# Optimization experiments

Measured on AMD Instinct MI355X. Metric: run time of the kernel, lower is better.

Reference implementation:

```python
import jax, jax.numpy as jnp
import numpy as np

B = 32          # batch_size
S = 64          # num_subgraph
D = 8           # dim_multi_hot (module-level global in source repo)
NE = S * D      # num_edges = 512
NNODES = 1024
E = 150000      # incidence rows
IN_UNITS = [16, 32, 32]
OUT_UNITS = [32, 32, 16]


def _glorot(key, shape):
    # glorot_normal over last two dims (out, in)
    fan_out, fan_in = shape[-2], shape[-1]
    std = (2.0 / (fan_in + fan_out)) ** 0.5
    return std * jax.random.normal(key, shape, dtype=jnp.float32)


def setup_inputs() -> dict:
    key = jax.random.key(0)
    ks = jax.random.split(key, 10)
    nodes_features = jax.random.normal(ks[0], (NNODES * S, IN_UNITS[0]), dtype=jnp.float32)
    c0 = jax.random.randint(ks[1], (E,), 0, B, dtype=jnp.int32)
    c1 = jax.random.randint(ks[2], (E,), 0, NNODES, dtype=jnp.int32)
    c2 = jax.random.randint(ks[3], (E,), 0, S, dtype=jnp.int32)
    c3 = jax.random.randint(ks[4], (E,), 0, D, dtype=jnp.int32)
    incidence_matrix = jnp.stack([c0, c1, c2, c3], axis=1)
    return {
        'nodes_features': nodes_features,
        'in_core0': _glorot(ks[5], (NE, IN_UNITS[1], IN_UNITS[0])),
        'in_bias0': jnp.zeros((NE, IN_UNITS[1], 1), jnp.float32),
        'in_core1': _glorot(ks[6], (NE, IN_UNITS[2], IN_UNITS[1])),
        'in_bias1': jnp.zeros((NE, IN_UNITS[2], 1), jnp.float32),
        'out_core0': _glorot(ks[7], (NE, OUT_UNITS[1], OUT_UNITS[0])),
        'out_bias0': jnp.zeros((NE, OUT_UNITS[1], 1), jnp.float32),
        'out_core1': _glorot(ks[8], (NE, OUT_UNITS[2], OUT_UNITS[1])),
        'out_bias1': jnp.zeros((NE, OUT_UNITS[2], 1), jnp.float32),
        'incidence_matrix': incidence_matrix,
    }


def reference(nodes_features, in_core0, in_bias0, in_core1, in_bias1,
              out_core0, out_bias0, out_core1, out_bias1, incidence_matrix):
    c0 = incidence_matrix[:, 0]
    c1 = incidence_matrix[:, 1]
    c2 = incidence_matrix[:, 2]
    c3 = incidence_matrix[:, 3]

    # gather node features per incidence row: [E, in0]
    x = nodes_features[c1 * S + c2]
    eidx = c2 * D + c3  # per-edge weight index, < NE

    # per-edge MLP (gathered batched matmul + bias + relu)
    for W, b in ((in_core0, in_bias0), (in_core1, in_bias1)):
        x = jax.nn.relu(jnp.einsum('eoi,ei->eo', W[eidx], x) + b[eidx, :, 0])

    # unsorted segment mean over irregular edge groups
    seg = c0 * (D * S) + c2 * D + c3
    nseg = B * S * D
    sums = jax.ops.segment_sum(x, seg, num_segments=nseg)           # [B*NE, 32]
    cnt = jax.ops.segment_sum(jnp.ones((x.shape[0], 1), x.dtype), seg, num_segments=nseg)
    ef = jnp.where(cnt > 0, sums / jnp.maximum(cnt, 1.0), 0.0)       # [B*NE, 32]

    # output MLP: weights tiled over batch (einsum avoids explicit repeat)
    ef = ef.reshape(B, NE, -1)
    for W, b in ((out_core0, out_bias0), (out_core1, out_bias1)):
        ef = jax.nn.relu(jnp.einsum('eoi,bei->beo', W, ef) + b[None, :, :, 0])

    return ef.reshape(B * NE, OUT_UNITS[-1], 1)
```

## Files before the change

kernel.cpp:

```cpp
#include <hip/hip_runtime.h>

#define B_    32
#define S_    64
#define D_    8
#define NE_   512
#define E_    150000
#define CAP   448
#define CSTRIDE 16

#define BMETA_BYTE_OFF   (NE_ * CSTRIDE * 4)
#define XSTAGE_BYTE_OFF  (BMETA_BYTE_OFF + NE_ * CAP * 4)

typedef __attribute__((ext_vector_type(8)))  short  short8;
typedef __attribute__((ext_vector_type(16))) float  float16;

__device__ __forceinline__ unsigned short f2bf(float f) {
    union { float f; unsigned int u; } cv; cv.f = f;
    unsigned int u = cv.u;
    return (unsigned short)((u + 0x7fffu + ((u >> 16) & 1u)) >> 16);
}
__device__ __forceinline__ unsigned int pack2bf(float a, float b) {
    return (unsigned int)f2bf(a) | ((unsigned int)f2bf(b) << 16);
}

__global__ __launch_bounds__(1024)
void scatter_stage_kernel(const int* __restrict__ inc,
                          const float* __restrict__ nf,
                          int* __restrict__ cursor,
                          int* __restrict__ bmeta,
                          uint4* __restrict__ xstage) {
    __shared__ int lcount[NE_];
    __shared__ int lbase[NE_];
    const int tid = threadIdx.x;

    for (int i = tid; i < NE_; i += 1024) lcount[i] = 0;
    __syncthreads();

    const int e = blockIdx.x * 1024 + tid;
    int ei = -1, lp = 0, b = 0, row = 0;
    if (e < E_) {
        const int4 c = ((const int4*)inc)[e];
        ei  = c.z * D_ + c.w;
        b   = c.x;
        row = c.y * S_ + c.z;
        lp  = atomicAdd(&lcount[ei], 1);
    }
    __syncthreads();
    for (int i = tid; i < NE_; i += 1024) {
        const int c = lcount[i];
        lbase[i] = (c > 0) ? atomicAdd(&cursor[i * CSTRIDE], c) : 0;
    }
    __syncthreads();
    if (ei >= 0) {
        const int idx = lbase[ei] + lp;
        if (idx < CAP) {
            const int slot = ei * CAP + idx;
            bmeta[slot] = b;
            const float4* xp = (const float4*)(nf + (size_t)row * 16);
            float4 v0 = xp[0], v1 = xp[1], v2 = xp[2], v3 = xp[3];
            uint4 pa, pb;
            pa.x = pack2bf(v0.x, v0.y); pa.y = pack2bf(v0.z, v0.w);
            pa.z = pack2bf(v1.x, v1.y); pa.w = pack2bf(v1.z, v1.w);
            pb.x = pack2bf(v2.x, v2.y); pb.y = pack2bf(v2.z, v2.w);
            pb.z = pack2bf(v3.x, v3.y); pb.w = pack2bf(v3.z, v3.w);
            xstage[slot * 2]     = pa;
            xstage[slot * 2 + 1] = pb;
        }
    }
}

#define HLP 40

__global__ __launch_bounds__(512, 4)
void main_mfma(const float* __restrict__ iw0, const float* __restrict__ ib0,
               const float* __restrict__ iw1, const float* __restrict__ ib1,
               const float* __restrict__ ow0, const float* __restrict__ ob0,
               const float* __restrict__ ow1, const float* __restrict__ ob1,
               const int* __restrict__ cursor, const int* __restrict__ bmeta,
               const uint4* __restrict__ xstage,
               float* __restrict__ out) {
    const int bid  = blockIdx.x;
    const int tid  = threadIdx.x;
    const int lane = tid & 63;
    const int wav  = tid >> 6;
    const int e32  = lane & 31;
    const int q    = lane >> 5;

    __shared__ float acc[32][33];
    __shared__ float hb[32][33];
    __shared__ float cnts[32];
    __shared__ float q0t[32 * 33];
    __shared__ float q1t[32 * 17];
    __shared__ float qb0s[32], qb1s[16];
    __shared__ unsigned short Hl[8][32 * HLP];

    short8 aWa, aWb0, aWb1;
    {
        const float* wa = iw0 + (size_t)bid * 512 + e32 * 16 + q * 8;
        float4 u0 = ((const float4*)wa)[0], u1 = ((const float4*)wa)[1];
        unsigned int p[4] = { pack2bf(u0.x,u0.y), pack2bf(u0.z,u0.w),
                              pack2bf(u1.x,u1.y), pack2bf(u1.z,u1.w) };
        aWa = *(short8*)p;
    }
    {
        const float* wb = iw1 + (size_t)bid * 1024 + e32 * 32 + q * 8;
        float4 u0 = ((const float4*)wb)[0], u1 = ((const float4*)wb)[1];
        unsigned int p[4] = { pack2bf(u0.x,u0.y), pack2bf(u0.z,u0.w),
                              pack2bf(u1.x,u1.y), pack2bf(u1.z,u1.w) };
        aWb0 = *(short8*)p;
        const float* wb2 = wb + 16;
        float4 u2 = ((const float4*)wb2)[0], u3 = ((const float4*)wb2)[1];
        unsigned int p2[4] = { pack2bf(u2.x,u2.y), pack2bf(u2.z,u2.w),
                               pack2bf(u3.x,u3.y), pack2bf(u3.z,u3.w) };
        aWb1 = *(short8*)p2;
    }
    float ba_r[16], bb_r[16];
    #pragma unroll
    for (int r = 0; r < 16; ++r) {
        const int o_r = (r & 3) + 8 * (r >> 2) + 4 * q;
        ba_r[r] = ib0[bid * 32 + o_r];
        bb_r[r] = ib1[bid * 32 + o_r];
    }

    for (int i = tid; i < 1024; i += 512) {
        const int o = i >> 5, k = i & 31;
        q0t[k * 33 + o] = ow0[(size_t)bid * 1024 + i];
    }
    { const int o = tid >> 5, k = tid & 31;
      q1t[k * 17 + o] = ow1[(size_t)bid * 512 + tid]; }
    if (tid < 32) { qb0s[tid] = ob0[bid * 32 + tid]; cnts[tid] = 0.f; }
    else if (tid < 48) qb1s[tid - 32] = ob1[bid * 16 + (tid - 32)];
    for (int i = tid; i < 32 * 33; i += 512) ((float*)acc)[i] = 0.f;
    __syncthreads();

    const int n = min(cursor[bid * CSTRIDE], CAP);
    const int ntiles = (n + 31) >> 5;
    const uint4* Xs = xstage + (size_t)bid * CAP * 2;
    const int*   Bm = bmeta + bid * CAP;
    unsigned short* hl = Hl[wav];

    for (int t = wav; t < ntiles; t += 8) {
        const int slot  = t * 32 + e32;
        const bool valid = slot < n;
        const int cs    = valid ? slot : (n - 1);

        short8 bX = *(const short8*)&Xs[cs * 2 + q];
        const int b_e = Bm[cs];

        float16 c0;
        #pragma unroll
        for (int r = 0; r < 16; ++r) c0[r] = ba_r[r];
        c0 = __builtin_amdgcn_mfma_f32_32x32x16_bf16(aWa, bX, c0, 0, 0, 0);

        #pragma unroll
        for (int r = 0; r < 16; r += 2) {
            const int o_r = (r & 3) + 8 * (r >> 2) + 4 * q;
            const unsigned int pk = pack2bf(fmaxf(c0[r], 0.f), fmaxf(c0[r + 1], 0.f));
            *(unsigned int*)(hl + e32 * HLP + o_r) = pk;
        }

        short8 bH0 = *(const short8*)(hl + e32 * HLP + q * 8);
        short8 bH1 = *(const short8*)(hl + e32 * HLP + 16 + q * 8);
        float16 c1;
        #pragma unroll
        for (int r = 0; r < 16; ++r) c1[r] = bb_r[r];
        c1 = __builtin_amdgcn_mfma_f32_32x32x16_bf16(aWb0, bH0, c1, 0, 0, 0);
        c1 = __builtin_amdgcn_mfma_f32_32x32x16_bf16(aWb1, bH1, c1, 0, 0, 0);

        if (valid) {
            #pragma unroll
            for (int r = 0; r < 16; ++r) {
                const int o_r = (r & 3) + 8 * (r >> 2) + 4 * q;
                atomicAdd(&acc[b_e][o_r], fmaxf(c1[r], 0.f));
            }
            if (q == 0) atomicAdd(&cnts[b_e], 1.f);
        }
    }
    __syncthreads();

    {
        const int b  = tid >> 4;
        const int j  = tid & 15;
        const float cv  = cnts[b];
        const float inv = cv > 0.f ? 1.0f / cv : 0.0f;
        #pragma unroll
        for (int s = 0; s < 2; ++s) {
            const int oo = j * 2 + s;
            float d = 0.f;
            #pragma unroll
            for (int k = 0; k < 32; ++k) d = fmaf(q0t[k * 33 + oo], acc[b][k], d);
            hb[b][oo] = fmaxf(fmaf(d, inv, qb0s[oo]), 0.f);
        }
    }
    __syncthreads();

    {
        const int b = tid >> 4;
        const int o = tid & 15;
        float d = qb1s[o];
        #pragma unroll
        for (int k = 0; k < 32; ++k) d = fmaf(q1t[k * 17 + o], hb[b][k], d);
        out[((size_t)b * NE_ + bid) * 16 + o] = fmaxf(d, 0.f);
    }
}

extern "C" void kernel_launch(void* const* d_in, const int* in_sizes, int n_in,
                              void* d_out, int out_size, void* d_ws, size_t ws_size,
                              hipStream_t stream) {
    const float* nf  = (const float*)d_in[0];
    const float* iw0 = (const float*)d_in[1];
    const float* ib0 = (const float*)d_in[2];
    const float* iw1 = (const float*)d_in[3];
    const float* ib1 = (const float*)d_in[4];
    const float* ow0 = (const float*)d_in[5];
    const float* ob0 = (const float*)d_in[6];
    const float* ow1 = (const float*)d_in[7];
    const float* ob1 = (const float*)d_in[8];
    const int*   inc = (const int*)d_in[9];

    int*   cursor = (int*)d_ws;
    int*   bmeta  = (int*)((char*)d_ws + BMETA_BYTE_OFF);
    uint4* xstage = (uint4*)((char*)d_ws + XSTAGE_BYTE_OFF);

    hipMemsetAsync(cursor, 0, NE_ * CSTRIDE * 4, stream);
    scatter_stage_kernel<<<(E_ + 1023) / 1024, 1024, 0, stream>>>(
        inc, nf, cursor, bmeta, xstage);
    main_mfma<<<NE_, 512, 0, stream>>>(iw0, ib0, iw1, ib1, ow0, ob0, ow1, ob1,
                                       cursor, bmeta, xstage, (float*)d_out);
}
```

Measured before the change: 123.9 us.

## Defer node feature gather to main kernel, scatter only packed index payload

```diff
diff --git a/kernel.cpp b/kernel.cpp
--- a/kernel.cpp
+++ b/kernel.cpp
@@ -8,8 +8,7 @@
 #define CAP   448
 #define CSTRIDE 16
 
-#define BMETA_BYTE_OFF   (NE_ * CSTRIDE * 4)
-#define XSTAGE_BYTE_OFF  (BMETA_BYTE_OFF + NE_ * CAP * 4)
+#define PAYLOAD_BYTE_OFF (NE_ * CSTRIDE * 4)
 
 typedef __attribute__((ext_vector_type(8)))  short  short8;
 typedef __attribute__((ext_vector_type(16))) float  float16;
@@ -24,11 +23,9 @@
 }
 
 __global__ __launch_bounds__(1024)
-void scatter_stage_kernel(const int* __restrict__ inc,
-                          const float* __restrict__ nf,
-                          int* __restrict__ cursor,
-                          int* __restrict__ bmeta,
-                          uint4* __restrict__ xstage) {
+void scatter_light(const int* __restrict__ inc,
+                   int* __restrict__ cursor,
+                   int* __restrict__ payload) {
     __shared__ int lcount[NE_];
     __shared__ int lbase[NE_];
     const int tid = threadIdx.x;
@@ -37,13 +34,12 @@
     __syncthreads();
 
     const int e = blockIdx.x * 1024 + tid;
-    int ei = -1, lp = 0, b = 0, row = 0;
+    int ei = -1, lp = 0, pl = 0;
     if (e < E_) {
         const int4 c = ((const int4*)inc)[e];
-        ei  = c.z * D_ + c.w;
-        b   = c.x;
-        row = c.y * S_ + c.z;
-        lp  = atomicAdd(&lcount[ei], 1);
+        ei = c.z * D_ + c.w;
+        pl = (c.x << 16) | (c.y * S_ + c.z);
+        lp = atomicAdd(&lcount[ei], 1);
     }
     __syncthreads();
     for (int i = tid; i < NE_; i += 1024) {
@@ -53,31 +49,19 @@
     __syncthreads();
     if (ei >= 0) {
         const int idx = lbase[ei] + lp;
-        if (idx < CAP) {
-            const int slot = ei * CAP + idx;
-            bmeta[slot] = b;
-            const float4* xp = (const float4*)(nf + (size_t)row * 16);
-            float4 v0 = xp[0], v1 = xp[1], v2 = xp[2], v3 = xp[3];
-            uint4 pa, pb;
-            pa.x = pack2bf(v0.x, v0.y); pa.y = pack2bf(v0.z, v0.w);
-            pa.z = pack2bf(v1.x, v1.y); pa.w = pack2bf(v1.z, v1.w);
-            pb.x = pack2bf(v2.x, v2.y); pb.y = pack2bf(v2.z, v2.w);
-            pb.z = pack2bf(v3.x, v3.y); pb.w = pack2bf(v3.z, v3.w);
-            xstage[slot * 2]     = pa;
-            xstage[slot * 2 + 1] = pb;
-        }
+        if (idx < CAP) payload[ei * CAP + idx] = pl;
     }
 }
 
 #define HLP 40
 
 __global__ __launch_bounds__(512, 4)
-void main_mfma(const float* __restrict__ iw0, const float* __restrict__ ib0,
+void main_mfma(const float* __restrict__ nf,
+               const float* __restrict__ iw0, const float* __restrict__ ib0,
                const float* __restrict__ iw1, const float* __restrict__ ib1,
                const float* __restrict__ ow0, const float* __restrict__ ob0,
                const float* __restrict__ ow1, const float* __restrict__ ob1,
-               const int* __restrict__ cursor, const int* __restrict__ bmeta,
-               const uint4* __restrict__ xstage,
+               const int* __restrict__ cursor, const int* __restrict__ payload,
                float* __restrict__ out) {
     const int bid  = blockIdx.x;
     const int tid  = threadIdx.x;
@@ -92,6 +76,7 @@
     __shared__ float q0t[32 * 33];
     __shared__ float q1t[32 * 17];
     __shared__ float qb0s[32], qb1s[16];
+    __shared__ float bias0s[32], bias1s[32];
     __shared__ unsigned short Hl[8][32 * HLP];
 
     short8 aWa, aWb0, aWb1;
@@ -114,13 +99,6 @@
                                pack2bf(u3.x,u3.y), pack2bf(u3.z,u3.w) };
         aWb1 = *(short8*)p2;
     }
-    float ba_r[16], bb_r[16];
-    #pragma unroll
-    for (int r = 0; r < 16; ++r) {
-        const int o_r = (r & 3) + 8 * (r >> 2) + 4 * q;
-        ba_r[r] = ib0[bid * 32 + o_r];
-        bb_r[r] = ib1[bid * 32 + o_r];
-    }
 
     for (int i = tid; i < 1024; i += 512) {
         const int o = i >> 5, k = i & 31;
@@ -128,15 +106,16 @@
     }
     { const int o = tid >> 5, k = tid & 31;
       q1t[k * 17 + o] = ow1[(size_t)bid * 512 + tid]; }
-    if (tid < 32) { qb0s[tid] = ob0[bid * 32 + tid]; cnts[tid] = 0.f; }
-    else if (tid < 48) qb1s[tid - 32] = ob1[bid * 16 + (tid - 32)];
+    if (tid < 32)       { bias0s[tid] = ib0[bid * 32 + tid]; cnts[tid] = 0.f; }
+    else if (tid < 64)  bias1s[tid - 32] = ib1[bid * 32 + (tid - 32)];
+    else if (tid < 96)  qb0s[tid - 64] = ob0[bid * 32 + (tid - 64)];
+    else if (tid < 112) qb1s[tid - 96] = ob1[bid * 16 + (tid - 96)];
     for (int i = tid; i < 32 * 33; i += 512) ((float*)acc)[i] = 0.f;
     __syncthreads();
 
     const int n = min(cursor[bid * CSTRIDE], CAP);
     const int ntiles = (n + 31) >> 5;
-    const uint4* Xs = xstage + (size_t)bid * CAP * 2;
-    const int*   Bm = bmeta + bid * CAP;
+    const int* Pl = payload + bid * CAP;
     unsigned short* hl = Hl[wav];
 
     for (int t = wav; t < ntiles; t += 8) {
@@ -144,12 +123,25 @@
         const bool valid = slot < n;
         const int cs    = valid ? slot : (n - 1);
 
-        short8 bX = *(const short8*)&Xs[cs * 2 + q];
-        const int b_e = Bm[cs];
+        const int p   = Pl[cs];
+        const int b_e = p >> 16;
+        const int row = p & 0xFFFF;
+
+        short8 bX;
+        {
+            const float4* xp = (const float4*)(nf + (size_t)row * 16 + q * 8);
+            float4 u0 = xp[0], u1 = xp[1];
+            unsigned int pk[4] = { pack2bf(u0.x,u0.y), pack2bf(u0.z,u0.w),
+                                   pack2bf(u1.x,u1.y), pack2bf(u1.z,u1.w) };
+            bX = *(short8*)pk;
+        }
 
         float16 c0;
         #pragma unroll
-        for (int r = 0; r < 16; ++r) c0[r] = ba_r[r];
+        for (int r = 0; r < 16; ++r) {
+            const int o_r = (r & 3) + 8 * (r >> 2) + 4 * q;
+            c0[r] = bias0s[o_r];
+        }
         c0 = __builtin_amdgcn_mfma_f32_32x32x16_bf16(aWa, bX, c0, 0, 0, 0);
 
         #pragma unroll
@@ -163,7 +155,10 @@
         short8 bH1 = *(const short8*)(hl + e32 * HLP + 16 + q * 8);
         float16 c1;
         #pragma unroll
-        for (int r = 0; r < 16; ++r) c1[r] = bb_r[r];
+        for (int r = 0; r < 16; ++r) {
+            const int o_r = (r & 3) + 8 * (r >> 2) + 4 * q;
+            c1[r] = bias1s[o_r];
+        }
         c1 = __builtin_amdgcn_mfma_f32_32x32x16_bf16(aWb0, bH0, c1, 0, 0, 0);
         c1 = __builtin_amdgcn_mfma_f32_32x32x16_bf16(aWb1, bH1, c1, 0, 0, 0);
 
@@ -218,13 +213,11 @@
     const float* ob1 = (const float*)d_in[8];
     const int*   inc = (const int*)d_in[9];
 
-    int*   cursor = (int*)d_ws;
-    int*   bmeta  = (int*)((char*)d_ws + BMETA_BYTE_OFF);
-    uint4* xstage = (uint4*)((char*)d_ws + XSTAGE_BYTE_OFF);
+    int* cursor  = (int*)d_ws;
+    int* payload = (int*)((char*)d_ws + PAYLOAD_BYTE_OFF);
 
     hipMemsetAsync(cursor, 0, NE_ * CSTRIDE * 4, stream);
-    scatter_stage_kernel<<<(E_ + 1023) / 1024, 1024, 0, stream>>>(
-        inc, nf, cursor, bmeta, xstage);
-    main_mfma<<<NE_, 512, 0, stream>>>(iw0, ib0, iw1, ib1, ow0, ob0, ow1, ob1,
-                                       cursor, bmeta, xstage, (float*)d_out);
-}
+    scatter_light<<<(E_ + 1023) / 1024, 1024, 0, stream>>>(inc, cursor, payload);
+    main_mfma<<<NE_, 512, 0, stream>>>(nf, iw0, ib0, iw1, ib1, ow0, ob0, ow1, ob1,
+                                       cursor, payload, (float*)d_out);
+}
```

Result: faster. 118.6 us (-4.3%).
